# Optimization experiments

Hardware: AMD Instinct MI355X
Metric: run time of the kernel (lower is better)

The kernel has to match this reference:

```python
import jax, jax.numpy as jnp
import numpy as np

HARD_NUM = 700      # hardcoded self.hard_num in HardOIMLoss
OIM_SCALAR = 30.0   # oim_scalar init arg
N, D, P, Q = 4096, 256, 5532, 5000


def _l2norm(x):
    return x / jnp.linalg.norm(x, axis=-1, keepdims=True)


def setup_inputs() -> dict:
    key = jax.random.key(0)
    k1, k2, k3, k4, k5 = jax.random.split(key, 5)
    # OIM features and lookup tables are L2-normalized rows
    inputs = _l2norm(jax.random.normal(k1, (N, D), dtype=jnp.float32))
    lut = _l2norm(jax.random.normal(k2, (P, D), dtype=jnp.float32))
    cq = _l2norm(jax.random.normal(k3, (Q, D), dtype=jnp.float32))
    reliability = jax.random.uniform(k4, (P + Q,), dtype=jnp.float32)
    labels = jax.random.randint(k5, (N,), 0, P, dtype=jnp.int32)
    return {"inputs": inputs, "labels": labels, "lut": lut, "cq": cq,
            "reliability": reliability}


def reference(inputs, labels, lut, cq, reliability):
    # projected[n, c] = <inputs_n, table_c> * reliability_c ;  table = [lut; cq]
    table = jnp.concatenate([lut, cq], axis=0)            # [P+Q, D]
    projected = (inputs @ table.T) * reliability[None, :]  # [N, P+Q]
    C = projected.shape[1]
    # value at sorted-descending index HARD_NUM == (HARD_NUM+1)-th largest
    boundary = jax.lax.top_k(projected, HARD_NUM + 1)[0][:, -1]  # [N]
    hard_mask = projected >= boundary[:, None]
    label_mask = jnp.arange(C, dtype=labels.dtype)[None, :] == labels[:, None]
    mask = hard_mask | label_mask
    logits = jnp.where(mask, projected * OIM_SCALAR, -jnp.inf)
    # cross entropy (mean over rows); label column is always unmasked
    logZ = jax.scipy.special.logsumexp(logits, axis=1)
    tgt = jnp.take_along_axis(logits, labels[:, None].astype(jnp.int32), axis=1)[:, 0]
    return jnp.mean(logZ - tgt)
```

## Files before the change

kernel.cpp:

```cpp
#include <hip/hip_runtime.h>
#include <math.h>

#define N_ROWS 4096
#define DIM    256
#define P_SZ   5532
#define Q_SZ   5000
#define C_COLS 10532
#define TPAD   10624
#define PSTR   10624
#define NGR    (PSTR / 16)
#define K_SEL  701
#define SCALAR 30.0f
#define C2     (SCALAR * 1.4426950408889634f)

typedef __attribute__((ext_vector_type(8))) short   short8;
typedef __attribute__((ext_vector_type(4))) float   float4_t;
typedef __attribute__((ext_vector_type(4))) unsigned short ushort4_t;
typedef __attribute__((ext_vector_type(8))) unsigned short ushort8_t;
typedef __attribute__((ext_vector_type(4))) unsigned int  uint4_t;

__device__ __forceinline__ unsigned short f2bf(float f) {
    unsigned u = __float_as_uint(f);
    unsigned r = u + 0x7FFFu + ((u >> 16) & 1u);
    return (unsigned short)(r >> 16);
}
__device__ __forceinline__ float bf2f(unsigned short u) {
    return __uint_as_float((unsigned)u << 16);
}
__device__ __forceinline__ unsigned short key16(unsigned short u) {
    return (u & 0x8000u) ? (unsigned short)(~u) : (unsigned short)(u | 0x8000u);
}
__device__ __forceinline__ float key2f16(unsigned key) {
    unsigned short b = (key & 0x8000u) ? (unsigned short)(key & 0x7FFFu)
                                       : (unsigned short)(~key & 0xFFFFu);
    return bf2f(b);
}
__device__ __forceinline__ void gload16(const void* g, void* l) {
    __builtin_amdgcn_global_load_lds(
        (const __attribute__((address_space(1))) unsigned int*)g,
        (__attribute__((address_space(3))) unsigned int*)l, 16, 0, 0);
}

#define NIN_G  (N_ROWS * DIM / 4)
#define NTAB_G (TPAD * DIM / 4)

__global__ __launch_bounds__(256) void convert_bf16(
    const float* __restrict__ inputs, const float* __restrict__ lut,
    const float* __restrict__ cq, unsigned short* __restrict__ in_bf,
    unsigned short* __restrict__ tab_bf)
{
    const int g = blockIdx.x * 256 + threadIdx.x;
    if (g >= NIN_G + NTAB_G) return;
    float4_t v;
    unsigned short* dst;
    if (g < NIN_G) {
        v = *(const float4_t*)&inputs[(size_t)g * 4];
        dst = in_bf + (size_t)g * 4;
    } else {
        const int t = g - NIN_G;
        const int row = t >> 6;
        const int c4  = (t & 63) * 4;
        if (row < P_SZ)        v = *(const float4_t*)&lut[(size_t)row * DIM + c4];
        else if (row < C_COLS) v = *(const float4_t*)&cq[(size_t)(row - P_SZ) * DIM + c4];
        else                   v = (float4_t){0.f, 0.f, 0.f, 0.f};
        dst = tab_bf + (size_t)t * 4;
    }
    ushort4_t h = { f2bf(v.x), f2bf(v.y), f2bf(v.z), f2bf(v.w) };
    *(ushort4_t*)dst = h;
}

#define NWG_X 83
#define NWG_Y 32
#define NWG   (NWG_X * NWG_Y)
#define CSTR  132

__global__ __launch_bounds__(256) void gemm_proj(
    const unsigned short* __restrict__ in_bf,
    const unsigned short* __restrict__ tab_bf,
    const float* __restrict__ rel,
    unsigned short* __restrict__ proj)
{
    __shared__ __align__(16) unsigned short smem[128 * CSTR];
    unsigned short* At = smem;
    unsigned short* Bt = smem + 128 * 64;

    const int tid  = threadIdx.x;
    const int lane = tid & 63, wid = tid >> 6;
    const int wm = wid >> 1, wn = wid & 1;

    const int phys = blockIdx.x;
    const int wg   = (phys & 7) * (NWG / 8) + (phys >> 3);
    const int bx   = wg >> 5;
    const int by   = wg & 31;
    const int row0 = by * 128, col0 = bx * 128;

    float4_t acc[4][4];
    #pragma unroll
    for (int i = 0; i < 4; ++i)
        #pragma unroll
        for (int j = 0; j < 4; ++j)
            acc[i][j] = (float4_t){0.f, 0.f, 0.f, 0.f};

    for (int k0 = 0; k0 < DIM; k0 += 64) {
        #pragma unroll
        for (int it = 0; it < 4; ++it) {
            const int g  = it * 256 + tid;
            const int r  = g >> 3;
            const int kb = ((g & 7) * 16) ^ ((r & 7) << 4);
            gload16(in_bf  + (size_t)(row0 + r) * DIM + k0 + (kb >> 1),
                    (char*)At + g * 16);
            gload16(tab_bf + (size_t)(col0 + r) * DIM + k0 + (kb >> 1),
                    (char*)Bt + g * 16);
        }
        __syncthreads();

        #pragma unroll
        for (int kk = 0; kk < 2; ++kk) {
            const int krow = lane & 15;
            const int kb   = kk * 64 + ((lane >> 4) << 4);
            short8 af[4], bfr[4];
            #pragma unroll
            for (int i = 0; i < 4; ++i) {
                const int r = wm * 64 + i * 16 + krow;
                af[i] = *(const short8*)((const char*)At + (r * 128 + (kb ^ ((r & 7) << 4))));
            }
            #pragma unroll
            for (int j = 0; j < 4; ++j) {
                const int r = wn * 64 + j * 16 + krow;
                bfr[j] = *(const short8*)((const char*)Bt + (r * 128 + (kb ^ ((r & 7) << 4))));
            }
            #pragma unroll
            for (int i = 0; i < 4; ++i)
                #pragma unroll
                for (int j = 0; j < 4; ++j)
                    acc[i][j] = __builtin_amdgcn_mfma_f32_16x16x32_bf16(af[i], bfr[j], acc[i][j], 0, 0, 0);
        }
        __syncthreads();
    }

    const int lr = (lane >> 4) << 2;
    const int lc = lane & 15;
    #pragma unroll
    for (int j = 0; j < 4; ++j) {
        const int cl  = wn * 64 + j * 16 + lc;
        const int col = col0 + cl;
        const bool pad = (col >= C_COLS);
        const float rl = pad ? 0.f : rel[col];
        #pragma unroll
        for (int i = 0; i < 4; ++i) {
            const int rbase = wm * 64 + i * 16 + lr;
            #pragma unroll
            for (int rr = 0; rr < 4; ++rr)
                smem[(rbase + rr) * CSTR + cl] =
                    pad ? (unsigned short)0u : key16(f2bf(acc[i][j][rr] * rl));
        }
    }
    __syncthreads();
    #pragma unroll
    for (int it = 0; it < 8; ++it) {
        const int g = it * 256 + tid;
        const int r = g >> 4;
        const int c8 = (g & 15) * 8;
        *(ushort8_t*)(proj + (size_t)(row0 + r) * PSTR + col0 + c8) =
            *(const ushort8_t*)&smem[r * CSTR + c8];
    }
}

#define NCPY  16
#define SCAP  32
__global__ __launch_bounds__(256) void row_loss_kernel(
    const unsigned short* __restrict__ proj, const int* __restrict__ labels,
    float* __restrict__ row_loss)
{
    __shared__ unsigned h1[NCPY * 257];
    __shared__ unsigned short stash[SCAP * 256];
    __shared__ unsigned h2[256];
    __shared__ unsigned wsum[4];
    __shared__ float    fsum[4];
    __shared__ unsigned sel_bin, sel_k, sel_sub, ovf;

    const int tid = threadIdx.x, lane = tid & 63, wid = tid >> 6;
    const int row = blockIdx.x;
    const uint4_t* prow = (const uint4_t*)(proj + (size_t)row * PSTR);
    const unsigned cbase = (unsigned)(tid & (NCPY - 1)) * 257;

    for (int i = tid; i < NCPY * 257; i += 256) h1[i] = 0;
    h2[tid] = 0;
    if (tid == 0) ovf = 0;
    __syncthreads();

    const int tailv = (1280 + tid < NGR);
    uint4_t r0 = prow[tid];
    uint4_t r1 = prow[256 + tid];
    uint4_t r2 = prow[512 + tid];
    uint4_t r3 = prow[768 + tid];
    uint4_t r4 = prow[1024 + tid];
    uint4_t r5 = prow[tailv ? 1280 + tid : 1279];

    auto HB = [&](unsigned w) {
        atomicAdd(&h1[cbase + ((w >> 8) & 0xFFu)], 1u);
        atomicAdd(&h1[cbase + (w >> 24)], 1u);
    };
    #pragma unroll
    for (int d = 0; d < 4; ++d) HB(r0[d]);
    #pragma unroll
    for (int d = 0; d < 4; ++d) HB(r1[d]);
    #pragma unroll
    for (int d = 0; d < 4; ++d) HB(r2[d]);
    #pragma unroll
    for (int d = 0; d < 4; ++d) HB(r3[d]);
    #pragma unroll
    for (int d = 0; d < 4; ++d) HB(r4[d]);
    if (tailv) {
        #pragma unroll
        for (int d = 0; d < 4; ++d) HB(r5[d]);
    }
    __syncthreads();

    {
        unsigned c = 0;
        #pragma unroll
        for (int cp = 0; cp < NCPY; ++cp) c += h1[cp * 257 + tid];
        unsigned incl = c;
        #pragma unroll
        for (int off = 1; off < 64; off <<= 1) {
            const unsigned t = __shfl_down(incl, off, 64);
            if (lane + off < 64) incl += t;
        }
        if (lane == 0) wsum[wid] = incl;
        __syncthreads();
        unsigned above = incl - c;
        for (int w = wid + 1; w < 4; ++w) above += wsum[w];
        if (above < K_SEL && above + c >= K_SEL) {
            sel_bin = (unsigned)tid; sel_k = K_SEL - above;
        }
    }
    __syncthreads();
    const unsigned b1 = sel_bin;
    const unsigned k2 = sel_k;
    const unsigned kfloor = b1 << 8;
    __syncthreads();

    unsigned cnt = 0;
    auto ST = [&](unsigned key) {
        if (key >= kfloor) {
            if (cnt < SCAP) stash[cnt * 256 + tid] = (unsigned short)key;
            else ovf = 1u;
            ++cnt;
        }
    };
    auto SW = [&](uint4_t w) {
        #pragma unroll
        for (int d = 0; d < 4; ++d) { ST(w[d] & 0xFFFFu); ST(w[d] >> 16); }
    };
    SW(r0); SW(r1); SW(r2); SW(r3); SW(r4);
    if (tailv) SW(r5);
    __syncthreads();

    float s = 0.f;
    unsigned bkey;
    if (ovf == 0) {
        const unsigned kceil = kfloor + 256u;
        for (unsigned c = 0; c < cnt; ++c) {
            const unsigned key = stash[c * 256 + tid];
            if (key < kceil) atomicAdd(&h2[key & 0xFFu], 1u);
        }
        __syncthreads();
        {
            const unsigned c = h2[tid];
            unsigned incl = c;
            #pragma unroll
            for (int off = 1; off < 64; off <<= 1) {
                const unsigned t = __shfl_down(incl, off, 64);
                if (lane + off < 64) incl += t;
            }
            if (lane == 0) wsum[wid] = incl;
            __syncthreads();
            unsigned above = incl - c;
            for (int w = wid + 1; w < 4; ++w) above += wsum[w];
            if (above < k2 && above + c >= k2) sel_sub = (unsigned)tid;
        }
        __syncthreads();
        bkey = kfloor | sel_sub;
        for (unsigned c = 0; c < cnt; ++c) {
            const unsigned key = stash[c * 256 + tid];
            if (key >= bkey) s += exp2f(C2 * key2f16(key) - C2);
        }
    } else {
        auto SB = [&](unsigned w) {
            const unsigned lo = w & 0xFFFFu, hi = w >> 16;
            if ((lo >> 8) == b1) atomicAdd(&h2[lo & 0xFFu], 1u);
            if ((hi >> 8) == b1) atomicAdd(&h2[hi & 0xFFu], 1u);
        };
        SB(r0[0]); SB(r0[1]); SB(r0[2]); SB(r0[3]);
        SB(r1[0]); SB(r1[1]); SB(r1[2]); SB(r1[3]);
        SB(r2[0]); SB(r2[1]); SB(r2[2]); SB(r2[3]);
        SB(r3[0]); SB(r3[1]); SB(r3[2]); SB(r3[3]);
        SB(r4[0]); SB(r4[1]); SB(r4[2]); SB(r4[3]);
        if (tailv) { SB(r5[0]); SB(r5[1]); SB(r5[2]); SB(r5[3]); }
        __syncthreads();
        {
            const unsigned c = h2[tid];
            unsigned incl = c;
            #pragma unroll
            for (int off = 1; off < 64; off <<= 1) {
                const unsigned t = __shfl_down(incl, off, 64);
                if (lane + off < 64) incl += t;
            }
            if (lane == 0) wsum[wid] = incl;
            __syncthreads();
            unsigned above = incl - c;
            for (int w = wid + 1; w < 4; ++w) above += wsum[w];
            if (above < k2 && above + c >= k2) sel_sub = (unsigned)tid;
        }
        __syncthreads();
        bkey = kfloor | sel_sub;
        auto EX = [&](unsigned w) {
            const unsigned lo = w & 0xFFFFu, hi = w >> 16;
            if (lo >= bkey) s += exp2f(C2 * key2f16(lo) - C2);
            if (hi >= bkey) s += exp2f(C2 * key2f16(hi) - C2);
        };
        EX(r0[0]); EX(r0[1]); EX(r0[2]); EX(r0[3]);
        EX(r1[0]); EX(r1[1]); EX(r1[2]); EX(r1[3]);
        EX(r2[0]); EX(r2[1]); EX(r2[2]); EX(r2[3]);
        EX(r3[0]); EX(r3[1]); EX(r3[2]); EX(r3[3]);
        EX(r4[0]); EX(r4[1]); EX(r4[2]); EX(r4[3]);
        if (tailv) { EX(r5[0]); EX(r5[1]); EX(r5[2]); EX(r5[3]); }
    }

    #pragma unroll
    for (int off = 1; off < 64; off <<= 1) {
        const float t = __shfl_down(s, off, 64);
        if (lane + off < 64) s += t;
    }
    if (lane == 0) fsum[wid] = s;
    __syncthreads();

    if (tid == 0) {
        float total = fsum[0] + fsum[1] + fsum[2] + fsum[3];
        const unsigned ulk = ((const unsigned short*)prow)[labels[row]];
        const float pl = key2f16(ulk);
        if (ulk < bkey) total += exp2f(C2 * pl - C2);
        row_loss[row] = SCALAR * 1.0f + logf(total) - SCALAR * pl;
    }
}

__global__ __launch_bounds__(256) void final_reduce(
    const float* __restrict__ row_loss, float* __restrict__ out)
{
    __shared__ float fred[4];
    const int tid = threadIdx.x, lane = tid & 63, wid = tid >> 6;
    float s = 0.f;
    for (int i = tid; i < N_ROWS; i += 256) s += row_loss[i];
    #pragma unroll
    for (int off = 1; off < 64; off <<= 1) {
        const float t = __shfl_down(s, off, 64);
        if (lane + off < 64) s += t;
    }
    if (lane == 0) fred[wid] = s;
    __syncthreads();
    if (tid == 0) out[0] = (fred[0] + fred[1] + fred[2] + fred[3]) / (float)N_ROWS;
}

extern "C" void kernel_launch(void* const* d_in, const int* in_sizes, int n_in,
                              void* d_out, int out_size, void* d_ws, size_t ws_size,
                              hipStream_t stream) {
    const float* inputs = (const float*)d_in[0];
    const int*   labels = (const int*)d_in[1];
    const float* lut    = (const float*)d_in[2];
    const float* cq     = (const float*)d_in[3];
    const float* rel    = (const float*)d_in[4];
    float* out = (float*)d_out;

    unsigned short* in_bf  = (unsigned short*)d_ws;
    unsigned short* tab_bf = in_bf  + (size_t)N_ROWS * DIM;
    unsigned short* proj   = tab_bf + (size_t)TPAD * DIM;
    float* rl_buf = (float*)(proj + (size_t)N_ROWS * PSTR);

    convert_bf16<<<(NIN_G + NTAB_G) / 256, 256, 0, stream>>>(inputs, lut, cq, in_bf, tab_bf);
    gemm_proj<<<NWG, 256, 0, stream>>>(in_bf, tab_bf, rel, proj);
    row_loss_kernel<<<N_ROWS, 256, 0, stream>>>(proj, labels, rl_buf);
    final_reduce<<<1, 256, 0, stream>>>(rl_buf, out);
}
```

Measured before the change: 100.2 us.

## Replace first-level LDS atomic histogram with register binary search over high byte

The first radix-select level no longer builds a 16-copy shared-memory histogram with atomics. It now runs an 8-pass binary search on the top byte, counting in registers how many keys meet each threshold, followed by wave and block reductions. This removes the LDS atomic contention and the histogram clearing and merging. In exchange it adds eight passes of compares over roughly 40 keys per thread and one barrier per pass. The freed shared memory may also allow more blocks per CU.

```diff
diff --git a/kernel.cpp b/kernel.cpp
--- a/kernel.cpp
+++ b/kernel.cpp
@@ -166,28 +166,23 @@
     }
 }
 
-#define NCPY  16
 #define SCAP  32
 __global__ __launch_bounds__(256) void row_loss_kernel(
     const unsigned short* __restrict__ proj, const int* __restrict__ labels,
     float* __restrict__ row_loss)
 {
-    __shared__ unsigned h1[NCPY * 257];
     __shared__ unsigned short stash[SCAP * 256];
     __shared__ unsigned h2[256];
-    __shared__ unsigned wsum[4];
+    __shared__ unsigned wsum[2][4];
     __shared__ float    fsum[4];
-    __shared__ unsigned sel_bin, sel_k, sel_sub, ovf;
+    __shared__ unsigned sel_sub, ovf;
 
     const int tid = threadIdx.x, lane = tid & 63, wid = tid >> 6;
     const int row = blockIdx.x;
     const uint4_t* prow = (const uint4_t*)(proj + (size_t)row * PSTR);
-    const unsigned cbase = (unsigned)(tid & (NCPY - 1)) * 257;
-
-    for (int i = tid; i < NCPY * 257; i += 256) h1[i] = 0;
+
     h2[tid] = 0;
     if (tid == 0) ovf = 0;
-    __syncthreads();
 
     const int tailv = (1280 + tid < NGR);
     uint4_t r0 = prow[tid];
@@ -197,49 +192,45 @@
     uint4_t r4 = prow[1024 + tid];
     uint4_t r5 = prow[tailv ? 1280 + tid : 1279];
 
-    auto HB = [&](unsigned w) {
-        atomicAdd(&h1[cbase + ((w >> 8) & 0xFFu)], 1u);
-        atomicAdd(&h1[cbase + (w >> 24)], 1u);
-    };
-    #pragma unroll
-    for (int d = 0; d < 4; ++d) HB(r0[d]);
-    #pragma unroll
-    for (int d = 0; d < 4; ++d) HB(r1[d]);
-    #pragma unroll
-    for (int d = 0; d < 4; ++d) HB(r2[d]);
-    #pragma unroll
-    for (int d = 0; d < 4; ++d) HB(r3[d]);
-    #pragma unroll
-    for (int d = 0; d < 4; ++d) HB(r4[d]);
-    if (tailv) {
-        #pragma unroll
-        for (int d = 0; d < 4; ++d) HB(r5[d]);
-    }
-    __syncthreads();
-
-    {
+    unsigned lo = 0, hi = 256, cnt_hi = 0;
+    for (int pass = 0; pass < 8; ++pass) {
+        const unsigned mid = (lo + hi) >> 1;
+        const unsigned hiT = mid << 24;
         unsigned c = 0;
-        #pragma unroll
-        for (int cp = 0; cp < NCPY; ++cp) c += h1[cp * 257 + tid];
-        unsigned incl = c;
+        auto CW = [&](unsigned w) {
+            c += (w >= hiT) ? 1u : 0u;
+            c += ((w << 16) >= hiT) ? 1u : 0u;
+        };
+        #pragma unroll
+        for (int d = 0; d < 4; ++d) CW(r0[d]);
+        #pragma unroll
+        for (int d = 0; d < 4; ++d) CW(r1[d]);
+        #pragma unroll
+        for (int d = 0; d < 4; ++d) CW(r2[d]);
+        #pragma unroll
+        for (int d = 0; d < 4; ++d) CW(r3[d]);
+        #pragma unroll
+        for (int d = 0; d < 4; ++d) CW(r4[d]);
+        if (tailv) {
+            #pragma unroll
+            for (int d = 0; d < 4; ++d) CW(r5[d]);
+        }
         #pragma unroll
         for (int off = 1; off < 64; off <<= 1) {
-            const unsigned t = __shfl_down(incl, off, 64);
-            if (lane + off < 64) incl += t;
-        }
-        if (lane == 0) wsum[wid] = incl;
-        __syncthreads();
-        unsigned above = incl - c;
-        for (int w = wid + 1; w < 4; ++w) above += wsum[w];
-        if (above < K_SEL && above + c >= K_SEL) {
-            sel_bin = (unsigned)tid; sel_k = K_SEL - above;
-        }
-    }
-    __syncthreads();
-    const unsigned b1 = sel_bin;
-    const unsigned k2 = sel_k;
+            const unsigned t = __shfl_down(c, off, 64);
+            if (lane + off < 64) c += t;
+        }
+        if (lane == 0) wsum[pass & 1][wid] = c;
+        __syncthreads();
+        const unsigned total = wsum[pass & 1][0] + wsum[pass & 1][1]
+                             + wsum[pass & 1][2] + wsum[pass & 1][3];
+        if (total >= K_SEL) lo = mid;
+        else { hi = mid; cnt_hi = total; }
+    }
+    const unsigned b1 = lo;
+    const unsigned k2 = K_SEL - cnt_hi;
     const unsigned kfloor = b1 << 8;
-    __syncthreads();
+    const unsigned kceil  = kfloor + 256u;
 
     unsigned cnt = 0;
     auto ST = [&](unsigned key) {
@@ -260,7 +251,6 @@
     float s = 0.f;
     unsigned bkey;
     if (ovf == 0) {
-        const unsigned kceil = kfloor + 256u;
         for (unsigned c = 0; c < cnt; ++c) {
             const unsigned key = stash[c * 256 + tid];
             if (key < kceil) atomicAdd(&h2[key & 0xFFu], 1u);
@@ -274,10 +264,10 @@
                 const unsigned t = __shfl_down(incl, off, 64);
                 if (lane + off < 64) incl += t;
             }
-            if (lane == 0) wsum[wid] = incl;
+            if (lane == 0) wsum[0][wid] = incl;
             __syncthreads();
             unsigned above = incl - c;
-            for (int w = wid + 1; w < 4; ++w) above += wsum[w];
+            for (int w = wid + 1; w < 4; ++w) above += wsum[0][w];
             if (above < k2 && above + c >= k2) sel_sub = (unsigned)tid;
         }
         __syncthreads();
@@ -288,16 +278,24 @@
         }
     } else {
         auto SB = [&](unsigned w) {
-            const unsigned lo = w & 0xFFFFu, hi = w >> 16;
-            if ((lo >> 8) == b1) atomicAdd(&h2[lo & 0xFFu], 1u);
-            if ((hi >> 8) == b1) atomicAdd(&h2[hi & 0xFFu], 1u);
+            const unsigned lv = w & 0xFFFFu, hv = w >> 16;
+            if ((lv >> 8) == b1) atomicAdd(&h2[lv & 0xFFu], 1u);
+            if ((hv >> 8) == b1) atomicAdd(&h2[hv & 0xFFu], 1u);
         };
-        SB(r0[0]); SB(r0[1]); SB(r0[2]); SB(r0[3]);
-        SB(r1[0]); SB(r1[1]); SB(r1[2]); SB(r1[3]);
-        SB(r2[0]); SB(r2[1]); SB(r2[2]); SB(r2[3]);
-        SB(r3[0]); SB(r3[1]); SB(r3[2]); SB(r3[3]);
-        SB(r4[0]); SB(r4[1]); SB(r4[2]); SB(r4[3]);
-        if (tailv) { SB(r5[0]); SB(r5[1]); SB(r5[2]); SB(r5[3]); }
+        #pragma unroll
+        for (int d = 0; d < 4; ++d) SB(r0[d]);
+        #pragma unroll
+        for (int d = 0; d < 4; ++d) SB(r1[d]);
+        #pragma unroll
+        for (int d = 0; d < 4; ++d) SB(r2[d]);
+        #pragma unroll
+        for (int d = 0; d < 4; ++d) SB(r3[d]);
+        #pragma unroll
+        for (int d = 0; d < 4; ++d) SB(r4[d]);
+        if (tailv) {
+            #pragma unroll
+            for (int d = 0; d < 4; ++d) SB(r5[d]);
+        }
         __syncthreads();
         {
             const unsigned c = h2[tid];
@@ -307,25 +305,33 @@
                 const unsigned t = __shfl_down(incl, off, 64);
                 if (lane + off < 64) incl += t;
             }
-            if (lane == 0) wsum[wid] = incl;
+            if (lane == 0) wsum[0][wid] = incl;
             __syncthreads();
             unsigned above = incl - c;
-            for (int w = wid + 1; w < 4; ++w) above += wsum[w];
+            for (int w = wid + 1; w < 4; ++w) above += wsum[0][w];
             if (above < k2 && above + c >= k2) sel_sub = (unsigned)tid;
         }
         __syncthreads();
         bkey = kfloor | sel_sub;
         auto EX = [&](unsigned w) {
-            const unsigned lo = w & 0xFFFFu, hi = w >> 16;
-            if (lo >= bkey) s += exp2f(C2 * key2f16(lo) - C2);
-            if (hi >= bkey) s += exp2f(C2 * key2f16(hi) - C2);
+            const unsigned lv = w & 0xFFFFu, hv = w >> 16;
+            if (lv >= bkey) s += exp2f(C2 * key2f16(lv) - C2);
+            if (hv >= bkey) s += exp2f(C2 * key2f16(hv) - C2);
         };
-        EX(r0[0]); EX(r0[1]); EX(r0[2]); EX(r0[3]);
-        EX(r1[0]); EX(r1[1]); EX(r1[2]); EX(r1[3]);
-        EX(r2[0]); EX(r2[1]); EX(r2[2]); EX(r2[3]);
-        EX(r3[0]); EX(r3[1]); EX(r3[2]); EX(r3[3]);
-        EX(r4[0]); EX(r4[1]); EX(r4[2]); EX(r4[3]);
-        if (tailv) { EX(r5[0]); EX(r5[1]); EX(r5[2]); EX(r5[3]); }
+        #pragma unroll
+        for (int d = 0; d < 4; ++d) EX(r0[d]);
+        #pragma unroll
+        for (int d = 0; d < 4; ++d) EX(r1[d]);
+        #pragma unroll
+        for (int d = 0; d < 4; ++d) EX(r2[d]);
+        #pragma unroll
+        for (int d = 0; d < 4; ++d) EX(r3[d]);
+        #pragma unroll
+        for (int d = 0; d < 4; ++d) EX(r4[d]);
+        if (tailv) {
+            #pragma unroll
+            for (int d = 0; d < 4; ++d) EX(r5[d]);
+        }
     }
 
     #pragma unroll
```

Measured after the change: 97.42 us. -2.7%, faster.
